# Kernel tuning notes

Measured on AMD Instinct MI355X. Metric: run time of the kernel, lower is better.

Reference implementation:

```python
import jax, jax.numpy as jnp
import numpy as np

B, T, D = 2, 2048, 1024
N, H = 16, 64  # num_heads, head_dim


def setup_inputs() -> dict:
    key = jax.random.key(0)
    ks = jax.random.split(key, 8)
    glorot = lambda k, shape, fan_in, fan_out: jax.random.uniform(
        k, shape, jnp.float32, -1.0, 1.0) * np.sqrt(6.0 / (fan_in + fan_out))
    return {
        "q": jax.random.normal(ks[0], (B, T, D), jnp.float32),
        "v": jax.random.normal(ks[1], (B, T, D), jnp.float32),
        "k": jax.random.normal(ks[2], (B, T, D), jnp.float32),
        "w_query": glorot(ks[3], (D, N, H), D, N * H),
        "b_query": jnp.zeros((N, 1, H), jnp.float32),
        "w_value": glorot(ks[4], (D, N, H), D, N * H),
        "b_value": jnp.zeros((N, 1, H), jnp.float32),
        "w_key": glorot(ks[5], (D, N, H), D, N * H),
        "b_key": jnp.zeros((N, 1, H), jnp.float32),
        "w_projection": glorot(ks[6], (N, D, H), N * H, D),
        "b_projection": jnp.zeros((1, D), jnp.float32),
    }


def reference(q, v, k, w_query, b_query, w_value, b_value, w_key, b_key,
              w_projection, b_projection):
    # QKV projections: [B,T,D] x [D,N,H] -> [B,N,T,H]
    query = jnp.einsum('btd,dnh->bnth', q, w_query) + b_query
    value = jnp.einsum('btd,dnh->bnth', v, w_value) + b_value
    key_p = jnp.einsum('btd,dnh->bnth', k, w_key) + b_key
    # Scaled dot-product attention, scores divided by sqrt(head_dim)
    scale = 1.0 / jnp.sqrt(jnp.asarray(H, query.dtype))
    scores = jnp.einsum('bnth,bnsh->bnts', query, key_p) * scale  # [B,N,T,T]
    weights = jax.nn.softmax(scores, axis=-1)
    attn = jnp.einsum('bnts,bnsh->bnth', weights, value)
    # Output projection: [B,N,T,H] x [N,D,H] -> [B,T,D]
    out = jnp.einsum('bnth,ndh->btd', attn, w_projection) + b_projection
    return out
```

## Files before the change

kernel.cpp:

```cpp
#include <hip/hip_runtime.h>
#include <hip/hip_bf16.h>
#include <cstdint>
#include <cstddef>


typedef __attribute__((ext_vector_type(8))) short short8;
typedef __attribute__((ext_vector_type(4))) float floatx4;
typedef __attribute__((ext_vector_type(8))) unsigned short ushort8;

#define EXP2F(x) __builtin_amdgcn_exp2f(x)

static __device__ __forceinline__ unsigned short f2bf(float f) {
    union { float f; unsigned int u; } v; v.f = f;
    unsigned int r = v.u + 0x7fffu + ((v.u >> 16) & 1u);
    return (unsigned short)(r >> 16);
}
static __device__ __forceinline__ unsigned int pk2bf(float lo, float hi) {
    __hip_bfloat162 t = __float22bfloat162_rn(make_float2(lo, hi));
    union { __hip_bfloat162 h; unsigned int u; } c; c.h = t;
    return c.u;
}
static __device__ __forceinline__ void gl_lds16(const unsigned short* g, unsigned short* l) {
    __builtin_amdgcn_global_load_lds(
        (const __attribute__((address_space(1))) unsigned int*)g,
        (__attribute__((address_space(3))) unsigned int*)l, 16, 0, 0);
}

__global__ __launch_bounds__(256) void mha_transpose_w(
    const float* __restrict__ wq, const float* __restrict__ wk, const float* __restrict__ wv,
    unsigned short* __restrict__ wqT, unsigned short* __restrict__ wkT, unsigned short* __restrict__ wvT)
{
    __shared__ float tile[32][33];
    const float* src; unsigned short* dst;
    int z = blockIdx.z;
    if (z == 0)      { src = wq; dst = wqT; }
    else if (z == 1) { src = wk; dst = wkT; }
    else             { src = wv; dst = wvT; }
    int n0 = blockIdx.x * 32, d0 = blockIdx.y * 32;
    int tx = threadIdx.x, ty = threadIdx.y;
    #pragma unroll
    for (int j = 0; j < 4; ++j)
        tile[ty + j * 8][tx] = src[(size_t)(d0 + ty + j * 8) * 1024 + n0 + tx];
    __syncthreads();
    #pragma unroll
    for (int j = 0; j < 4; ++j)
        dst[(size_t)(n0 + ty + j * 8) * 1024 + d0 + tx] = f2bf(tile[tx][ty + j * 8]);
}

__global__ __launch_bounds__(256) void mha_reorder_wp(
    const float* __restrict__ wp, unsigned short* __restrict__ wp2)
{
    int base = blockIdx.x * 1024 + threadIdx.x;
    #pragma unroll
    for (int i = 0; i < 4; ++i) {
        int idx = base + i * 256;
        int n = idx >> 16, d = (idx >> 6) & 1023, h = idx & 63;
        wp2[(size_t)d * 1024 + n * 64 + h] = f2bf(wp[idx]);
    }
}

__global__ __launch_bounds__(256) void prep_bf16_3(
    const float* __restrict__ x0, const float* __restrict__ x1, const float* __restrict__ x2,
    unsigned short* __restrict__ o0, unsigned short* __restrict__ o1, unsigned short* __restrict__ o2)
{
    int y = blockIdx.y;
    const float* x = y == 0 ? x0 : (y == 1 ? x1 : x2);
    unsigned short* o = y == 0 ? o0 : (y == 1 ? o1 : o2);
    size_t i = ((size_t)blockIdx.x * 256 + threadIdx.x) * 8;
    float4 a = *(const float4*)(x + i);
    float4 b = *(const float4*)(x + i + 4);
    uint4 pk;
    pk.x = pk2bf(a.x, a.y); pk.y = pk2bf(a.z, a.w);
    pk.z = pk2bf(b.x, b.y); pk.w = pk2bf(b.z, b.w);
    *(uint4*)(o + i) = pk;
}

__global__ __launch_bounds__(256) void mha_tr_v(
    const unsigned short* __restrict__ Vp, unsigned short* __restrict__ Vt)
{
    __shared__ unsigned short tile[64][72];
    int bn = blockIdx.x, tb = blockIdx.y;
    int tid = threadIdx.x;
    const unsigned short* src = Vp + ((size_t)bn * 2048 + tb * 64) * 64;
    unsigned short* dst = Vt + (size_t)bn * 64 * 2048 + tb * 64;
    int r = tid >> 2, cq = (tid & 3) * 16;
    *(ushort8*)&tile[r][cq]     = *(const ushort8*)(src + r * 64 + cq);
    *(ushort8*)&tile[r][cq + 8] = *(const ushort8*)(src + r * 64 + cq + 8);
    __syncthreads();
    int h = tid >> 2, t0 = (tid & 3) * 16;
    ushort8 o0, o1;
    #pragma unroll
    for (int j = 0; j < 8; ++j) { o0[j] = tile[t0 + j][h]; o1[j] = tile[t0 + 8 + j][h]; }
    *(ushort8*)(dst + (size_t)h * 2048 + t0)     = o0;
    *(ushort8*)(dst + (size_t)h * 2048 + t0 + 8) = o1;
}

__global__ __launch_bounds__(256) void gemm_qkv128(
    const unsigned short* __restrict__ A0, const unsigned short* __restrict__ A1,
    const unsigned short* __restrict__ A2,
    const unsigned short* __restrict__ W0, const unsigned short* __restrict__ W1,
    const unsigned short* __restrict__ W2,
    const float* __restrict__ b0, const float* __restrict__ b1, const float* __restrict__ b2,
    unsigned short* __restrict__ O0, unsigned short* __restrict__ O1, unsigned short* __restrict__ O2,
    float qscale, int matSel, int scatterV)
{
    __shared__ unsigned short As[128 * 32];
    __shared__ unsigned short Bs[128 * 32];
    int mat, nt, bm;
    if (matSel < 0) {
        int g = blockIdx.x + (blockIdx.y << 5);
        int xcd = g & 7, s = g >> 3;
        int grp = xcd * 3 + (s >> 5);
        bm = s & 31;
        mat = grp >> 3; nt = grp & 7;
    } else { mat = matSel; nt = blockIdx.y; bm = blockIdx.x; }
    const unsigned short* A  = mat == 0 ? A0 : (mat == 1 ? A1 : A2);
    const unsigned short* WT = mat == 0 ? W0 : (mat == 1 ? W1 : W2);
    const float* bias        = mat == 0 ? b0 : (mat == 1 ? b1 : b2);
    unsigned short* Out      = mat == 0 ? O0 : (mat == 1 ? O1 : O2);
    float scale = (mat == 0) ? qscale : 1.0f;
    int vmode = (mat == 2) && scatterV;

    int tid = threadIdx.x;
    int w = tid >> 6, lane = tid & 63, c15 = lane & 15, quad = lane >> 4;
    int wm = w >> 1, wn = w & 1;

    const unsigned short* gA[2]; unsigned short* lA[2];
    const unsigned short* gB[2]; unsigned short* lB[2];
    #pragma unroll
    for (int i = 0; i < 2; ++i) {
        int s = (w * 2 + i) * 64 + lane;
        gA[i] = A  + (size_t)(bm * 128 + (s >> 2)) * 1024 + (s & 3) * 8;
        lA[i] = &As[s * 8];
        gB[i] = WT + (size_t)(nt * 128 + (s >> 2)) * 1024 + (s & 3) * 8;
        lB[i] = &Bs[s * 8];
    }

    floatx4 acc[4][4];
    #pragma unroll
    for (int mi = 0; mi < 4; ++mi)
        #pragma unroll
        for (int ni = 0; ni < 4; ++ni) acc[mi][ni] = (floatx4){0.f, 0.f, 0.f, 0.f};

    for (int kt = 0; kt < 32; ++kt) {
        __syncthreads();
        #pragma unroll
        for (int i = 0; i < 2; ++i) { gl_lds16(gA[i] + kt * 32, lA[i]); gl_lds16(gB[i] + kt * 32, lB[i]); }
        __syncthreads();
        short8 af[4], bfr[4];
        #pragma unroll
        for (int mi = 0; mi < 4; ++mi)
            af[mi] = *(const short8*)&As[(wm * 64 + mi * 16 + c15) * 32 + quad * 8];
        #pragma unroll
        for (int ni = 0; ni < 4; ++ni)
            bfr[ni] = *(const short8*)&Bs[(wn * 64 + ni * 16 + c15) * 32 + quad * 8];
        #pragma unroll
        for (int mi = 0; mi < 4; ++mi)
            #pragma unroll
            for (int ni = 0; ni < 4; ++ni)
                acc[mi][ni] = __builtin_amdgcn_mfma_f32_16x16x32_bf16(af[mi], bfr[ni], acc[mi][ni], 0, 0, 0);
    }
    #pragma unroll
    for (int mi = 0; mi < 4; ++mi)
        #pragma unroll
        for (int ni = 0; ni < 4; ++ni)
            #pragma unroll
            for (int r = 0; r < 4; ++r) {
                int row = bm * 128 + wm * 64 + mi * 16 + quad * 4 + r;
                int col = nt * 128 + wn * 64 + ni * 16 + c15;
                float val = (acc[mi][ni][r] + bias[col]) * scale;
                int b = row >> 11, t = row & 2047, n = col >> 6, h = col & 63;
                if (vmode)
                    Out[((size_t)(b * 16 + n) * 64 + h) * 2048 + t] = f2bf(val);
                else
                    Out[((size_t)(b * 16 + n) * 2048 + t) * 64 + h] = f2bf(val);
            }
}

__global__ __launch_bounds__(256) void mha_flash3(
    const unsigned short* __restrict__ Qp, const unsigned short* __restrict__ Kp,
    const unsigned short* __restrict__ Vt, unsigned short* __restrict__ attnb)
{
    __shared__ unsigned short Ks[64 * 72];
    __shared__ unsigned short Vs[64 * 72];
    __shared__ unsigned short Pl[4][32 * 72];

    int bi = blockIdx.x;
    int xcd = bi & 7, j = bi >> 3;
    int bn = xcd * 4 + (j >> 4), qt = j & 15;
    int b = bn >> 4, n = bn & 15;
    int tid = threadIdx.x;
    int w = tid >> 6, lane = tid & 63, c15 = lane & 15, quad = lane >> 4;

    const unsigned short* Qb = Qp + (size_t)bn * 2048 * 64;
    const unsigned short* Kb = Kp + (size_t)bn * 2048 * 64;
    const unsigned short* Vb = Vt + (size_t)bn * 64 * 2048;

    int qbase = qt * 128 + w * 32;

    short8 bQ[2][2];
    #pragma unroll
    for (int tni = 0; tni < 2; ++tni)
        #pragma unroll
        for (int kc = 0; kc < 2; ++kc)
            bQ[tni][kc] = *(const short8*)(Qb + (size_t)(qbase + tni * 16 + c15) * 64 + kc * 32 + quad * 8);

    float l_i[2] = {0.f, 0.f};
    floatx4 o[2][4];
    #pragma unroll
    for (int i = 0; i < 2; ++i)
        #pragma unroll
        for (int j2 = 0; j2 < 4; ++j2) o[i][j2] = (floatx4){0.f, 0.f, 0.f, 0.f};

    unsigned short* Pw = &Pl[w][0];
    int srow = tid >> 3, scc = tid & 7;

    ushort8 kreg[2], vreg[2];
    #pragma unroll
    for (int i = 0; i < 2; ++i) {
        kreg[i] = *(const ushort8*)(Kb + (size_t)(srow + i * 32) * 64 + scc * 8);
        vreg[i] = *(const ushort8*)(Vb + (size_t)(srow + i * 32) * 2048 + scc * 8);
    }

    for (int it = 0; it < 32; ++it) {
        __syncthreads();
        #pragma unroll
        for (int i = 0; i < 2; ++i) {
            *(ushort8*)&Ks[(srow + i * 32) * 72 + scc * 8] = kreg[i];
            *(ushort8*)&Vs[(srow + i * 32) * 72 + scc * 8] = vreg[i];
        }
        if (it < 31) {
            int s1 = (it + 1) * 64;
            #pragma unroll
            for (int i = 0; i < 2; ++i) {
                kreg[i] = *(const ushort8*)(Kb + (size_t)(s1 + srow + i * 32) * 64 + scc * 8);
                vreg[i] = *(const ushort8*)(Vb + (size_t)(srow + i * 32) * 2048 + s1 + scc * 8);
            }
        }
        __syncthreads();

        floatx4 sc[4][2];
        __builtin_amdgcn_s_setprio(1);
        #pragma unroll
        for (int smi = 0; smi < 4; ++smi) {
            short8 a0 = *(const short8*)&Ks[(smi * 16 + c15) * 72 + quad * 8];
            short8 a1 = *(const short8*)&Ks[(smi * 16 + c15) * 72 + 32 + quad * 8];
            #pragma unroll
            for (int tni = 0; tni < 2; ++tni) {
                floatx4 t = (floatx4){0.f, 0.f, 0.f, 0.f};
                t = __builtin_amdgcn_mfma_f32_16x16x32_bf16(a0, bQ[tni][0], t, 0, 0, 0);
                t = __builtin_amdgcn_mfma_f32_16x16x32_bf16(a1, bQ[tni][1], t, 0, 0, 0);
                sc[smi][tni] = t;
            }
        }
        __builtin_amdgcn_s_setprio(0);
        #pragma unroll
        for (int tni = 0; tni < 2; ++tni) {
            float rs = 0.f;
            #pragma unroll
            for (int smi = 0; smi < 4; ++smi) {
                float p0 = EXP2F(sc[smi][tni][0]);
                float p1 = EXP2F(sc[smi][tni][1]);
                float p2 = EXP2F(sc[smi][tni][2]);
                float p3 = EXP2F(sc[smi][tni][3]);
                rs += (p0 + p1) + (p2 + p3);
                uint2 pw;
                pw.x = pk2bf(p0, p1);
                pw.y = pk2bf(p2, p3);
                *(uint2*)&Pw[(tni * 16 + c15) * 72 + smi * 16 + quad * 4] = pw;
            }
            l_i[tni] += rs;
        }
        short8 bv[4][2];
        #pragma unroll
        for (int hni = 0; hni < 4; ++hni)
            #pragma unroll
            for (int kc = 0; kc < 2; ++kc)
                bv[hni][kc] = *(const short8*)&Vs[(hni * 16 + c15) * 72 + kc * 32 + quad * 8];
        __builtin_amdgcn_s_setprio(1);
        #pragma unroll
        for (int tmi = 0; tmi < 2; ++tmi) {
            short8 ap0 = *(const short8*)&Pw[(tmi * 16 + c15) * 72 + quad * 8];
            short8 ap1 = *(const short8*)&Pw[(tmi * 16 + c15) * 72 + 32 + quad * 8];
            #pragma unroll
            for (int hni = 0; hni < 4; ++hni) {
                o[tmi][hni] = __builtin_amdgcn_mfma_f32_16x16x32_bf16(ap0, bv[hni][0], o[tmi][hni], 0, 0, 0);
                o[tmi][hni] = __builtin_amdgcn_mfma_f32_16x16x32_bf16(ap1, bv[hni][1], o[tmi][hni], 0, 0, 0);
            }
        }
        __builtin_amdgcn_s_setprio(0);
    }
    float lf[2];
    #pragma unroll
    for (int tmi = 0; tmi < 2; ++tmi) {
        float s = l_i[tmi];
        s += __shfl_xor(s, 16, 64);
        s += __shfl_xor(s, 32, 64);
        lf[tmi] = s;
    }
    #pragma unroll
    for (int tmi = 0; tmi < 2; ++tmi)
        #pragma unroll
        for (int r = 0; r < 4; ++r) {
            float linv = 1.0f / __shfl(lf[tmi], quad * 4 + r, 64);
            int t = qbase + tmi * 16 + quad * 4 + r;
            #pragma unroll
            for (int hni = 0; hni < 4; ++hni) {
                int col = n * 64 + hni * 16 + c15;
                attnb[(size_t)(b * 2048 + t) * 1024 + col] = f2bf(o[tmi][hni][r] * linv);
            }
        }
}

__global__ __launch_bounds__(256) void gemm_out64v2(
    const unsigned short* __restrict__ A, const unsigned short* __restrict__ BT,
    const float* __restrict__ bias, float* __restrict__ out)
{
    __shared__ unsigned short As[64 * 64];
    __shared__ unsigned short Bs[128 * 64];
    int g = blockIdx.x + (blockIdx.y << 6);
    int nt = g & 7, bm = g >> 3;
    int tid = threadIdx.x;
    int w = tid >> 6, lane = tid & 63, c15 = lane & 15, quad = lane >> 4;
    int wm = w >> 1, wn = w & 1;

    const unsigned short* gA[2]; unsigned short* lA[2];
    const unsigned short* gB[4]; unsigned short* lB[4];
    #pragma unroll
    for (int i = 0; i < 2; ++i) {
        int s = (w * 2 + i) * 64 + lane;
        int row = s >> 3, cl = (s & 7) ^ (row & 7);
        gA[i] = A + (size_t)(bm * 64 + row) * 1024 + cl * 8;
        lA[i] = &As[s * 8];
    }
    #pragma unroll
    for (int i = 0; i < 4; ++i) {
        int s = (w * 4 + i) * 64 + lane;
        int row = s >> 3, cl = (s & 7) ^ (row & 7);
        gB[i] = BT + (size_t)(nt * 128 + row) * 1024 + cl * 8;
        lB[i] = &Bs[s * 8];
    }

    floatx4 acc[2][4];
    #pragma unroll
    for (int mi = 0; mi < 2; ++mi)
        #pragma unroll
        for (int ni = 0; ni < 4; ++ni) acc[mi][ni] = (floatx4){0.f, 0.f, 0.f, 0.f};

    for (int kt = 0; kt < 16; ++kt) {
        __syncthreads();
        #pragma unroll
        for (int i = 0; i < 2; ++i) gl_lds16(gA[i] + kt * 64, lA[i]);
        #pragma unroll
        for (int i = 0; i < 4; ++i) gl_lds16(gB[i] + kt * 64, lB[i]);
        __syncthreads();
        #pragma unroll
        for (int kc = 0; kc < 2; ++kc) {
            short8 af[2], bfr[4];
            #pragma unroll
            for (int mi = 0; mi < 2; ++mi) {
                int row = wm * 32 + mi * 16 + c15;
                af[mi] = *(const short8*)&As[row * 64 + (((kc * 4 + quad) ^ (row & 7)) * 8)];
            }
            #pragma unroll
            for (int ni = 0; ni < 4; ++ni) {
                int row = wn * 64 + ni * 16 + c15;
                bfr[ni] = *(const short8*)&Bs[row * 64 + (((kc * 4 + quad) ^ (row & 7)) * 8)];
            }
            #pragma unroll
            for (int mi = 0; mi < 2; ++mi)
                #pragma unroll
                for (int ni = 0; ni < 4; ++ni)
                    acc[mi][ni] = __builtin_amdgcn_mfma_f32_16x16x32_bf16(af[mi], bfr[ni], acc[mi][ni], 0, 0, 0);
        }
    }
    #pragma unroll
    for (int mi = 0; mi < 2; ++mi)
        #pragma unroll
        for (int ni = 0; ni < 4; ++ni)
            #pragma unroll
            for (int r = 0; r < 4; ++r) {
                int row = bm * 64 + wm * 32 + mi * 16 + quad * 4 + r;
                int col = nt * 128 + wn * 64 + ni * 16 + c15;
                out[(size_t)row * 1024 + col] = acc[mi][ni][r] + bias[col];
            }
}

extern "C" void kernel_launch(void* const* d_in, const int* in_sizes, int n_in,
                              void* d_out, int out_size, void* d_ws, size_t ws_size,
                              hipStream_t stream)
{
    const float* q  = (const float*)d_in[0];
    const float* v  = (const float*)d_in[1];
    const float* k  = (const float*)d_in[2];
    const float* wq = (const float*)d_in[3];
    const float* bq = (const float*)d_in[4];
    const float* wv = (const float*)d_in[5];
    const float* bv = (const float*)d_in[6];
    const float* wk = (const float*)d_in[7];
    const float* bk = (const float*)d_in[8];
    const float* wp = (const float*)d_in[9];
    const float* bp = (const float*)d_in[10];
    float* out = (float*)d_out;

    char* ws = (char*)d_ws;
    unsigned short* wqT  = (unsigned short*)(ws + (size_t)0);
    unsigned short* wkT  = (unsigned short*)(ws + ((size_t)2  << 20));
    unsigned short* wvT  = (unsigned short*)(ws + ((size_t)4  << 20));
    unsigned short* wp2  = (unsigned short*)(ws + ((size_t)6  << 20));
    unsigned short* Qp   = (unsigned short*)(ws + ((size_t)8  << 20));
    unsigned short* Kp   = (unsigned short*)(ws + ((size_t)16 << 20));
    unsigned short* Vtp  = (unsigned short*)(ws + ((size_t)24 << 20));
    unsigned short* Xb   = (unsigned short*)(ws + ((size_t)32 << 20));
    unsigned short* attnb= (unsigned short*)(ws + ((size_t)32 << 20));

    const float qscale = 0.125f * 1.44269504088896f;

    hipLaunchKernelGGL(mha_transpose_w, dim3(32, 32, 3), dim3(32, 8), 0, stream,
                       wq, wk, wv, wqT, wkT, wvT);
    hipLaunchKernelGGL(mha_reorder_wp, dim3(1024), dim3(256), 0, stream, wp, wp2);

    if (ws_size >= ((size_t)64 << 20)) {
        unsigned short* qb = (unsigned short*)(ws + ((size_t)40 << 20));
        unsigned short* kb = (unsigned short*)(ws + ((size_t)48 << 20));
        unsigned short* vb = (unsigned short*)(ws + ((size_t)56 << 20));
        unsigned short* Vp = Xb;
        hipLaunchKernelGGL(prep_bf16_3, dim3(2048, 3), dim3(256), 0, stream, q, k, v, qb, kb, vb);
        hipLaunchKernelGGL(gemm_qkv128, dim3(32, 24), dim3(256), 0, stream,
                           qb, kb, vb, wqT, wkT, wvT, bq, bk, bv, Qp, Kp, Vp, qscale, -1, 0);
        hipLaunchKernelGGL(mha_tr_v, dim3(32, 32), dim3(256), 0, stream, Vp, Vtp);
    } else {
        hipLaunchKernelGGL(prep_bf16_3, dim3(2048, 1), dim3(256), 0, stream, q, q, q, Xb, Xb, Xb);
        hipLaunchKernelGGL(gemm_qkv128, dim3(32, 8), dim3(256), 0, stream,
                           Xb, Xb, Xb, wqT, wkT, wvT, bq, bk, bv, Qp, Kp, Vtp, qscale, 0, 1);
        hipLaunchKernelGGL(prep_bf16_3, dim3(2048, 1), dim3(256), 0, stream, k, k, k, Xb, Xb, Xb);
        hipLaunchKernelGGL(gemm_qkv128, dim3(32, 8), dim3(256), 0, stream,
                           Xb, Xb, Xb, wqT, wkT, wvT, bq, bk, bv, Qp, Kp, Vtp, qscale, 1, 1);
        hipLaunchKernelGGL(prep_bf16_3, dim3(2048, 1), dim3(256), 0, stream, v, v, v, Xb, Xb, Xb);
        hipLaunchKernelGGL(gemm_qkv128, dim3(32, 8), dim3(256), 0, stream,
                           Xb, Xb, Xb, wqT, wkT, wvT, bq, bk, bv, Qp, Kp, Vtp, qscale, 2, 1);
    }

    hipLaunchKernelGGL(mha_flash3, dim3(512), dim3(256), 0, stream, Qp, Kp, Vtp, attnb);
    hipLaunchKernelGGL(gemm_out64v2, dim3(64, 8), dim3(256), 0, stream, attnb, wp2, bp, out);
}
```

Baseline: 231.8 us.

## Fuse fp32-to-bf16 input conversion into QKV GEMM and drop setprio hints

Removes the separate prep_bf16_3 conversion kernel. The QKV GEMM now loads fp32 activations directly into registers, prefetched one k-step ahead, and converts them to bf16 while writing to LDS. This saves a kernel launch and the write and re-read of the bf16 intermediate, but the GEMM now reads twice as many A bytes and replaces async global-to-LDS loads with register staging. It also drops the XCD-aware block remapping and the low-workspace fallback path, and removes the s_setprio hints around the MFMA sections in the flash kernel.

```diff
diff --git a/kernel.cpp b/kernel.cpp
--- a/kernel.cpp
+++ b/kernel.cpp
@@ -57,22 +57,6 @@
         int n = idx >> 16, d = (idx >> 6) & 1023, h = idx & 63;
         wp2[(size_t)d * 1024 + n * 64 + h] = f2bf(wp[idx]);
     }
-}
-
-__global__ __launch_bounds__(256) void prep_bf16_3(
-    const float* __restrict__ x0, const float* __restrict__ x1, const float* __restrict__ x2,
-    unsigned short* __restrict__ o0, unsigned short* __restrict__ o1, unsigned short* __restrict__ o2)
-{
-    int y = blockIdx.y;
-    const float* x = y == 0 ? x0 : (y == 1 ? x1 : x2);
-    unsigned short* o = y == 0 ? o0 : (y == 1 ? o1 : o2);
-    size_t i = ((size_t)blockIdx.x * 256 + threadIdx.x) * 8;
-    float4 a = *(const float4*)(x + i);
-    float4 b = *(const float4*)(x + i + 4);
-    uint4 pk;
-    pk.x = pk2bf(a.x, a.y); pk.y = pk2bf(a.z, a.w);
-    pk.z = pk2bf(b.x, b.y); pk.w = pk2bf(b.z, b.w);
-    *(uint4*)(o + i) = pk;
 }
 
 __global__ __launch_bounds__(256) void mha_tr_v(
@@ -96,41 +80,33 @@
 }
 
 __global__ __launch_bounds__(256) void gemm_qkv128(
-    const unsigned short* __restrict__ A0, const unsigned short* __restrict__ A1,
-    const unsigned short* __restrict__ A2,
+    const float* __restrict__ A0, const float* __restrict__ A1, const float* __restrict__ A2,
     const unsigned short* __restrict__ W0, const unsigned short* __restrict__ W1,
     const unsigned short* __restrict__ W2,
     const float* __restrict__ b0, const float* __restrict__ b1, const float* __restrict__ b2,
     unsigned short* __restrict__ O0, unsigned short* __restrict__ O1, unsigned short* __restrict__ O2,
-    float qscale, int matSel, int scatterV)
+    float qscale)
 {
     __shared__ unsigned short As[128 * 32];
     __shared__ unsigned short Bs[128 * 32];
-    int mat, nt, bm;
-    if (matSel < 0) {
-        int g = blockIdx.x + (blockIdx.y << 5);
-        int xcd = g & 7, s = g >> 3;
-        int grp = xcd * 3 + (s >> 5);
-        bm = s & 31;
-        mat = grp >> 3; nt = grp & 7;
-    } else { mat = matSel; nt = blockIdx.y; bm = blockIdx.x; }
-    const unsigned short* A  = mat == 0 ? A0 : (mat == 1 ? A1 : A2);
+    int bm = blockIdx.x, by = blockIdx.y;
+    int mat = by >> 3, nt = by & 7;
+    const float* A           = mat == 0 ? A0 : (mat == 1 ? A1 : A2);
     const unsigned short* WT = mat == 0 ? W0 : (mat == 1 ? W1 : W2);
     const float* bias        = mat == 0 ? b0 : (mat == 1 ? b1 : b2);
     unsigned short* Out      = mat == 0 ? O0 : (mat == 1 ? O1 : O2);
     float scale = (mat == 0) ? qscale : 1.0f;
-    int vmode = (mat == 2) && scatterV;
 
     int tid = threadIdx.x;
     int w = tid >> 6, lane = tid & 63, c15 = lane & 15, quad = lane >> 4;
     int wm = w >> 1, wn = w & 1;
 
-    const unsigned short* gA[2]; unsigned short* lA[2];
+    const float* gAf[2]; unsigned short* lA[2];
     const unsigned short* gB[2]; unsigned short* lB[2];
     #pragma unroll
     for (int i = 0; i < 2; ++i) {
         int s = (w * 2 + i) * 64 + lane;
-        gA[i] = A  + (size_t)(bm * 128 + (s >> 2)) * 1024 + (s & 3) * 8;
+        gAf[i] = A + (size_t)(bm * 128 + (s >> 2)) * 1024 + (s & 3) * 8;
         lA[i] = &As[s * 8];
         gB[i] = WT + (size_t)(nt * 128 + (s >> 2)) * 1024 + (s & 3) * 8;
         lB[i] = &Bs[s * 8];
@@ -142,10 +118,32 @@
         #pragma unroll
         for (int ni = 0; ni < 4; ++ni) acc[mi][ni] = (floatx4){0.f, 0.f, 0.f, 0.f};
 
+    float4 af4[2][2];
+    #pragma unroll
+    for (int i = 0; i < 2; ++i) {
+        af4[i][0] = *(const float4*)(gAf[i]);
+        af4[i][1] = *(const float4*)(gAf[i] + 4);
+    }
+
     for (int kt = 0; kt < 32; ++kt) {
         __syncthreads();
         #pragma unroll
-        for (int i = 0; i < 2; ++i) { gl_lds16(gA[i] + kt * 32, lA[i]); gl_lds16(gB[i] + kt * 32, lB[i]); }
+        for (int i = 0; i < 2; ++i) {
+            gl_lds16(gB[i] + kt * 32, lB[i]);
+            uint4 pk;
+            pk.x = pk2bf(af4[i][0].x, af4[i][0].y);
+            pk.y = pk2bf(af4[i][0].z, af4[i][0].w);
+            pk.z = pk2bf(af4[i][1].x, af4[i][1].y);
+            pk.w = pk2bf(af4[i][1].z, af4[i][1].w);
+            *(uint4*)lA[i] = pk;
+        }
+        if (kt < 31) {
+            #pragma unroll
+            for (int i = 0; i < 2; ++i) {
+                af4[i][0] = *(const float4*)(gAf[i] + (kt + 1) * 32);
+                af4[i][1] = *(const float4*)(gAf[i] + (kt + 1) * 32 + 4);
+            }
+        }
         __syncthreads();
         short8 af[4], bfr[4];
         #pragma unroll
@@ -170,10 +168,7 @@
                 int col = nt * 128 + wn * 64 + ni * 16 + c15;
                 float val = (acc[mi][ni][r] + bias[col]) * scale;
                 int b = row >> 11, t = row & 2047, n = col >> 6, h = col & 63;
-                if (vmode)
-                    Out[((size_t)(b * 16 + n) * 64 + h) * 2048 + t] = f2bf(val);
-                else
-                    Out[((size_t)(b * 16 + n) * 2048 + t) * 64 + h] = f2bf(val);
+                Out[((size_t)(b * 16 + n) * 2048 + t) * 64 + h] = f2bf(val);
             }
 }
 
@@ -240,7 +235,6 @@
         __syncthreads();
 
         floatx4 sc[4][2];
-        __builtin_amdgcn_s_setprio(1);
         #pragma unroll
         for (int smi = 0; smi < 4; ++smi) {
             short8 a0 = *(const short8*)&Ks[(smi * 16 + c15) * 72 + quad * 8];
@@ -253,7 +247,6 @@
                 sc[smi][tni] = t;
             }
         }
-        __builtin_amdgcn_s_setprio(0);
         #pragma unroll
         for (int tni = 0; tni < 2; ++tni) {
             float rs = 0.f;
@@ -277,7 +270,6 @@
             #pragma unroll
             for (int kc = 0; kc < 2; ++kc)
                 bv[hni][kc] = *(const short8*)&Vs[(hni * 16 + c15) * 72 + kc * 32 + quad * 8];
-        __builtin_amdgcn_s_setprio(1);
         #pragma unroll
         for (int tmi = 0; tmi < 2; ++tmi) {
             short8 ap0 = *(const short8*)&Pw[(tmi * 16 + c15) * 72 + quad * 8];
@@ -288,7 +280,6 @@
                 o[tmi][hni] = __builtin_amdgcn_mfma_f32_16x16x32_bf16(ap1, bv[hni][1], o[tmi][hni], 0, 0, 0);
             }
         }
-        __builtin_amdgcn_s_setprio(0);
     }
     float lf[2];
     #pragma unroll
@@ -411,7 +402,7 @@
     unsigned short* Qp   = (unsigned short*)(ws + ((size_t)8  << 20));
     unsigned short* Kp   = (unsigned short*)(ws + ((size_t)16 << 20));
     unsigned short* Vtp  = (unsigned short*)(ws + ((size_t)24 << 20));
-    unsigned short* Xb   = (unsigned short*)(ws + ((size_t)32 << 20));
+    unsigned short* Vp   = (unsigned short*)(ws + ((size_t)32 << 20));
     unsigned short* attnb= (unsigned short*)(ws + ((size_t)32 << 20));
 
     const float qscale = 0.125f * 1.44269504088896f;
@@ -420,26 +411,9 @@
                        wq, wk, wv, wqT, wkT, wvT);
     hipLaunchKernelGGL(mha_reorder_wp, dim3(1024), dim3(256), 0, stream, wp, wp2);
 
-    if (ws_size >= ((size_t)64 << 20)) {
-        unsigned short* qb = (unsigned short*)(ws + ((size_t)40 << 20));
-        unsigned short* kb = (unsigned short*)(ws + ((size_t)48 << 20));
-        unsigned short* vb = (unsigned short*)(ws + ((size_t)56 << 20));
-        unsigned short* Vp = Xb;
-        hipLaunchKernelGGL(prep_bf16_3, dim3(2048, 3), dim3(256), 0, stream, q, k, v, qb, kb, vb);
-        hipLaunchKernelGGL(gemm_qkv128, dim3(32, 24), dim3(256), 0, stream,
-                           qb, kb, vb, wqT, wkT, wvT, bq, bk, bv, Qp, Kp, Vp, qscale, -1, 0);
-        hipLaunchKernelGGL(mha_tr_v, dim3(32, 32), dim3(256), 0, stream, Vp, Vtp);
-    } else {
-        hipLaunchKernelGGL(prep_bf16_3, dim3(2048, 1), dim3(256), 0, stream, q, q, q, Xb, Xb, Xb);
-        hipLaunchKernelGGL(gemm_qkv128, dim3(32, 8), dim3(256), 0, stream,
-                           Xb, Xb, Xb, wqT, wkT, wvT, bq, bk, bv, Qp, Kp, Vtp, qscale, 0, 1);
-        hipLaunchKernelGGL(prep_bf16_3, dim3(2048, 1), dim3(256), 0, stream, k, k, k, Xb, Xb, Xb);
-        hipLaunchKernelGGL(gemm_qkv128, dim3(32, 8), dim3(256), 0, stream,
-                           Xb, Xb, Xb, wqT, wkT, wvT, bq, bk, bv, Qp, Kp, Vtp, qscale, 1, 1);
-        hipLaunchKernelGGL(prep_bf16_3, dim3(2048, 1), dim3(256), 0, stream, v, v, v, Xb, Xb, Xb);
-        hipLaunchKernelGGL(gemm_qkv128, dim3(32, 8), dim3(256), 0, stream,
-                           Xb, Xb, Xb, wqT, wkT, wvT, bq, bk, bv, Qp, Kp, Vtp, qscale, 2, 1);
-    }
+    hipLaunchKernelGGL(gemm_qkv128, dim3(32, 24), dim3(256), 0, stream,
+                       q, k, v, wqT, wkT, wvT, bq, bk, bv, Qp, Kp, Vp, qscale);
+    hipLaunchKernelGGL(mha_tr_v, dim3(32, 32), dim3(256), 0, stream, Vp, Vtp);
 
     hipLaunchKernelGGL(mha_flash3, dim3(512), dim3(256), 0, stream, Qp, Kp, Vtp, attnb);
     hipLaunchKernelGGL(gemm_out64v2, dim3(64, 8), dim3(256), 0, stream, attnb, wp2, bp, out);
```

New measurement: 234.5 us. Within noise of the previous version (+1.2%).
